# Performance work log

Hardware: AMD Instinct MI355X
Metric: run time of the kernel (lower is better)

The kernel has to match this reference:

```python
import jax, jax.numpy as jnp
import numpy as np

N = 100000
E = 1600000
FEAT = 128
EMB = 64
HID = 64
OUT = 16


def _glorot(key, shape):
    fan_in, fan_out = shape[1], shape[0]
    lim = (6.0 / (fan_in + fan_out)) ** 0.5
    return jax.random.uniform(key, shape, jnp.float32, -lim, lim)


def setup_inputs() -> dict:
    key = jax.random.key(0)
    ks = jax.random.split(key, 16)
    return {
        "x_feat": jax.random.normal(ks[0], (N, FEAT), jnp.float32),
        "x_emb": jax.random.normal(ks[1], (N, 2, EMB), jnp.float32),
        "edge_index": jax.random.randint(ks[2], (2, E), 0, N, jnp.int32),
        # layer 0: SAGEConv(FEAT -> HID), Linear(EMB -> HID)
        "Wl0": _glorot(ks[3], (HID, FEAT)),
        "bl0": jnp.zeros((HID,), jnp.float32),
        "Wr0": _glorot(ks[4], (HID, FEAT)),
        "We0": _glorot(ks[5], (HID, EMB)),
        "be0": jnp.zeros((HID,), jnp.float32),
        # layer 1 (last): SAGEConv(HID -> OUT), Linear(EMB==HID -> OUT)
        "Wl1": _glorot(ks[6], (OUT, HID)),
        "bl1": jnp.zeros((OUT,), jnp.float32),
        "Wr1": _glorot(ks[7], (OUT, HID)),
        "We1": _glorot(ks[8], (OUT, HID)),
        "be1": jnp.zeros((OUT,), jnp.float32),
    }


def _sage_conv(x, edge_index, Wl, bl, Wr):
    # PyG SAGEConv with mean aggregation:
    #   out = lin_l(mean_{j in N(i)} x_j) + lin_r(x_i)
    src, dst = edge_index[0], edge_index[1]
    msg = x[src]                                   # [E, C] gather
    agg = jax.ops.segment_sum(msg, dst, num_segments=N)       # [N, C]
    deg = jax.ops.segment_sum(jnp.ones((E,), x.dtype), dst, num_segments=N)
    agg = agg / jnp.maximum(deg, 1.0)[:, None]     # mean over neighbors
    return agg @ Wl.T + bl + x @ Wr.T


def reference(x_feat, x_emb, edge_index,
              Wl0, bl0, Wr0, We0, be0,
              Wl1, bl1, Wr1, We1, be1):
    # forward(x=(x_feat, x_emb), edge_index=...) path, eval mode (dropout p=0)
    e = x_emb.mean(axis=1)                         # [N, EMB]
    # layer 0 (all but last): relu(sage + linear(emb))
    h = _sage_conv(x_feat, edge_index, Wl0, bl0, Wr0)
    e = e @ We0.T + be0
    h = jax.nn.relu(h + e)
    # last layer: no relu
    h = _sage_conv(h, edge_index, Wl1, bl1, Wr1)
    e = e @ We1.T + be1
    return h + e
```

## Files before the change

kernel.cpp:

```cpp
#include <hip/hip_runtime.h>
#include <hip/hip_bf16.h>
#include <cstddef>

#define NN 100000
#define EE 1600000
#define NPB 128
#define NB  782
#define ECH 4096
#define NCH 391
#define CAP 4096

typedef __attribute__((ext_vector_type(8))) short bf16x8;
typedef __attribute__((ext_vector_type(8))) unsigned short u16x8;
typedef __attribute__((ext_vector_type(4))) float f32x4;

#define YTS 72

static inline int ceil_div(int a, int b){ return (a + b - 1) / b; }

__device__ inline unsigned short f2bf(float f){
  union { float f; unsigned u; } v; v.f = f;
  unsigned r = (v.u + 0x7fff + ((v.u >> 16) & 1)) >> 16;
  return (unsigned short)r;
}
__device__ inline float bf2f(unsigned short s){
  union { unsigned u; float f; } v; v.u = ((unsigned)s) << 16;
  return v.f;
}

#define PRE_W (128 * 192)
#define PRE_E (PRE_W + 16 * 64)
#define PRE_B (PRE_E + 16)
#define PRE_C (PRE_B + 64)
#define PRE_N (PRE_C + NB)
__global__ void prep_all_kernel(const float* __restrict__ Wl0, const float* __restrict__ Wr0,
                                const float* __restrict__ We0, const float* __restrict__ bl0,
                                const float* __restrict__ be0, const float* __restrict__ We1,
                                const float* __restrict__ be1,
                                unsigned short* __restrict__ wcat, float* __restrict__ wee,
                                float* __restrict__ b1e, float* __restrict__ bias0,
                                int* __restrict__ cur){
  int idx = blockIdx.x * blockDim.x + threadIdx.x;
  if (idx < PRE_W){
    int n = idx / 192, k = idx % 192;
    float v;
    if (n < 64) v = (k < 128) ? Wl0[n * 128 + k] : 0.f;
    else        v = (k < 128) ? Wr0[(n - 64) * 128 + k] : We0[(n - 64) * 64 + (k - 128)];
    wcat[idx] = f2bf(v);
  } else if (idx < PRE_E){
    int j = idx - PRE_W;
    int i = j >> 6, c = j & 63;
    float s = 0.f;
    for (int k = 0; k < 64; k++) s += We1[i * 64 + k] * We0[k * 64 + c];
    wee[j] = s;
  } else if (idx < PRE_B){
    int i = idx - PRE_E;
    float s = be1[i];
    for (int k = 0; k < 64; k++) s += We1[i * 64 + k] * be0[k];
    b1e[i] = s;
  } else if (idx < PRE_C){
    int i = idx - PRE_B;
    bias0[i] = bl0[i] + be0[i];
  } else if (idx < PRE_N){
    cur[idx - PRE_C] = 0;
  }
}

__global__ __launch_bounds__(256) void escatter_kernel(const int* __restrict__ src,
                                                       const int* __restrict__ dst,
                                                       int* __restrict__ cur,
                                                       int* __restrict__ ebkt){
  __shared__ int lh[NB];
  __shared__ int lo[NB];
  int t = threadIdx.x;
  int e0 = blockIdx.x * ECH;
  int ne = EE - e0; if (ne > ECH) ne = ECH;
  for (int i = t; i < NB; i += 256) lh[i] = 0;
  __syncthreads();
  for (int i = t; i < ne; i += 256)
    atomicAdd(&lh[dst[e0 + i] >> 7], 1);
  __syncthreads();
  for (int i = t; i < NB; i += 256){
    int c = lh[i];
    lo[i] = c ? atomicAdd(&cur[i], c) : 0;
    lh[i] = 0;
  }
  __syncthreads();
  for (int i = t; i < ne; i += 256){
    int d = dst[e0 + i], b = d >> 7;
    int r = atomicAdd(&lh[b], 1);
    int p = lo[b] + r;
    if (p < CAP) ebkt[b * CAP + p] = ((d & 127) << 24) | src[e0 + i];
  }
}

__global__ __launch_bounds__(256) void bsort_kernel(
    const int* __restrict__ cur, int* __restrict__ ebkt,
    int* __restrict__ rs, int* __restrict__ deg){
  __shared__ int lraw[CAP];
  __shared__ int lout[CAP];
  __shared__ int lh[NPB];
  __shared__ int loff[NPB];
  __shared__ int lcur[NPB];
  const int t = threadIdx.x;
  const int b = blockIdx.x;
  const int e0 = b * CAP;
  int cnt = cur[b];
  if (cnt > CAP) cnt = CAP;
  for (int i = t; i < NPB; i += 256) lh[i] = 0;
  __syncthreads();
  for (int i = t; i < cnt; i += 256){
    int w = ebkt[e0 + i];
    lraw[i] = w;
    atomicAdd(&lh[((unsigned)w) >> 24], 1);
  }
  __syncthreads();
  {
    int v = (t < NPB) ? lh[t] : 0;
    int s = v;
    for (int off = 1; off < NPB; off <<= 1){
      int x = 0;
      if (t < NPB && t >= off) x = loff[t - off];
      __syncthreads();
      if (t < NPB) loff[t] = s;
      __syncthreads();
      if (t < NPB && t >= off) s += loff[t - off];
      __syncthreads();
    }
    if (t < NPB){ loff[t] = s - v; lcur[t] = s - v; }
  }
  __syncthreads();
  for (int i = t; i < cnt; i += 256){
    int w = lraw[i];
    int d = ((unsigned)w) >> 24;
    int pos = atomicAdd(&lcur[d], 1);
    lout[pos] = w & 0xFFFFFF;
  }
  __syncthreads();
  for (int i = t; i < cnt; i += 256) ebkt[e0 + i] = lout[i];
  if (t < NPB){
    int node = b * NPB + t;
    if (node < NN){
      rs[node]  = e0 + loff[t];
      deg[node] = lh[t];
    }
  }
}

__global__ __launch_bounds__(256, 4) void l0_gemm_kernel(
    const float* __restrict__ x_feat, const float* __restrict__ x_emb,
    const unsigned short* __restrict__ wcat,
    unsigned short* __restrict__ y0g, unsigned short* __restrict__ re0g,
    unsigned short* __restrict__ e_bf, int M){
  __shared__ unsigned short smem[64 * 200];
  unsigned short* As = smem;
  unsigned short* Ys = smem;
  unsigned short* Rs = smem + 64 * YTS;
  const int t = threadIdx.x;
  const int row0 = blockIdx.x * 64;
  float4 tmpa[12], tmpb[12];
  #pragma unroll
  for (int k = 0; k < 12; k++){
    int idx = t + k * 256;
    int r = idx / 48, q = idx % 48;
    int row = row0 + r;
    float4 v = make_float4(0.f, 0.f, 0.f, 0.f);
    float4 u = make_float4(0.f, 0.f, 0.f, 0.f);
    if (row < M){
      if (q < 32) v = ((const float4*)x_feat)[(size_t)row * 32 + q];
      else {
        v = ((const float4*)x_emb)[(size_t)row * 32 + (q - 32)];
        u = ((const float4*)x_emb)[(size_t)row * 32 + 16 + (q - 32)];
      }
    }
    tmpa[k] = v; tmpb[k] = u;
  }
  #pragma unroll
  for (int k = 0; k < 12; k++){
    int idx = t + k * 256;
    int r = idx / 48, q = idx % 48;
    int row = row0 + r;
    float4 v = tmpa[k];
    if (q >= 32){
      float4 u = tmpb[k];
      v.x = 0.5f * (v.x + u.x); v.y = 0.5f * (v.y + u.y);
      v.z = 0.5f * (v.z + u.z); v.w = 0.5f * (v.w + u.w);
    }
    ushort4 s; s.x = f2bf(v.x); s.y = f2bf(v.y); s.z = f2bf(v.z); s.w = f2bf(v.w);
    *(ushort4*)&As[r * 200 + q * 4] = s;
    if (q >= 32 && row < M)
      *(ushort4*)&e_bf[(size_t)row * 64 + (q - 32) * 4] = s;
  }
  const int w = t >> 6, l = t & 63;
  const int lm = l & 15, quad = l >> 4;
  bf16x8 bfr0[6], bfr1[6];
  {
    int n0 = w * 16 + lm;
    int n1 = 64 + w * 16 + lm;
    #pragma unroll
    for (int ks = 0; ks < 6; ks++){
      bfr0[ks] = *(const bf16x8*)&wcat[n0 * 192 + ks * 32 + quad * 8];
      bfr1[ks] = *(const bf16x8*)&wcat[n1 * 192 + ks * 32 + quad * 8];
    }
  }
  __syncthreads();
  f32x4 a0[4], a1[4];
  #pragma unroll
  for (int rg = 0; rg < 4; rg++){
    bf16x8 af[6];
    #pragma unroll
    for (int ks = 0; ks < 6; ks++)
      af[ks] = *(const bf16x8*)&As[(rg * 16 + lm) * 200 + ks * 32 + quad * 8];
    f32x4 acc0 = {0.f, 0.f, 0.f, 0.f};
    f32x4 acc1 = {0.f, 0.f, 0.f, 0.f};
    #pragma unroll
    for (int ks = 0; ks < 6; ks++){
      acc0 = __builtin_amdgcn_mfma_f32_16x16x32_bf16(af[ks], bfr0[ks], acc0, 0, 0, 0);
      acc1 = __builtin_amdgcn_mfma_f32_16x16x32_bf16(af[ks], bfr1[ks], acc1, 0, 0, 0);
    }
    a0[rg] = acc0; a1[rg] = acc1;
  }
  __syncthreads();
  #pragma unroll
  for (int rg = 0; rg < 4; rg++){
    #pragma unroll
    for (int r = 0; r < 4; r++){
      int lrow = rg * 16 + quad * 4 + r;
      Ys[lrow * YTS + w * 16 + lm] = f2bf(a0[rg][r]);
      Rs[lrow * YTS + w * 16 + lm] = f2bf(a1[rg][r]);
    }
  }
  __syncthreads();
  #pragma unroll
  for (int k = 0; k < 2; k++){
    int idx = t + k * 256;
    int r = idx >> 3, c8 = idx & 7;
    int grow = row0 + r;
    if (grow < M){
      *(u16x8*)&y0g[(size_t)grow * 64 + c8 * 8]  = *(const u16x8*)&Ys[r * YTS + c8 * 8];
      *(u16x8*)&re0g[(size_t)grow * 64 + c8 * 8] = *(const u16x8*)&Rs[r * YTS + c8 * 8];
    }
  }
}

__global__ void agg0_kernel(const unsigned short* __restrict__ y0,
                            const unsigned short* __restrict__ re0,
                            const float* __restrict__ bias0,
                            const int* __restrict__ rs, const int* __restrict__ deg,
                            const int* __restrict__ ssrc, unsigned short* __restrict__ h){
  int g = blockIdx.x * blockDim.x + threadIdx.x;
  if (g >= NN * 8) return;
  int node = g >> 3, lane = g & 7;
  int start = rs[node], cnt = deg[node];
  float acc[4][8] = {};
  int i = 0;
  for (; i + 8 <= cnt; i += 8){
    int s[8];
    #pragma unroll
    for (int j = 0; j < 8; j++) s[j] = ssrc[start + i + j];
    u16x8 v[8];
    #pragma unroll
    for (int j = 0; j < 8; j++) v[j] = *(const u16x8*)&y0[(size_t)s[j] * 64 + lane * 8];
    #pragma unroll
    for (int j = 0; j < 8; j++)
      #pragma unroll
      for (int k = 0; k < 8; k++) acc[j & 3][k] += bf2f((unsigned short)v[j][k]);
  }
  for (; i < cnt; i++){
    int s = ssrc[start + i];
    u16x8 v = *(const u16x8*)&y0[(size_t)s * 64 + lane * 8];
    #pragma unroll
    for (int k = 0; k < 8; k++) acc[0][k] += bf2f((unsigned short)v[k]);
  }
  float inv = 1.0f / (float)(cnt > 1 ? cnt : 1);
  u16x8 rv = *(const u16x8*)&re0[(size_t)node * 64 + lane * 8];
  float4 ba = ((const float4*)bias0)[lane * 2];
  float4 bb = ((const float4*)bias0)[lane * 2 + 1];
  float bv[8] = {ba.x, ba.y, ba.z, ba.w, bb.x, bb.y, bb.z, bb.w};
  u16x8 o;
  #pragma unroll
  for (int k = 0; k < 8; k++){
    float sum = (acc[0][k] + acc[1][k]) + (acc[2][k] + acc[3][k]);
    float x = sum * inv + bf2f((unsigned short)rv[k]) + bv[k];
    o[k] = f2bf(x > 0.f ? x : 0.f);
  }
  *(u16x8*)&h[(size_t)node * 64 + lane * 8] = o;
}

__global__ __launch_bounds__(256) void gemm16_dual_kernel(
    const unsigned short* __restrict__ H, const unsigned short* __restrict__ E,
    const float* __restrict__ Wl1, const float* __restrict__ Wr1,
    const float* __restrict__ wee,
    const float* __restrict__ bl1, const float* __restrict__ b1e,
    unsigned short* __restrict__ Y1, float* __restrict__ Out, int M){
  __shared__ float Hs[64][65];
  __shared__ float Es[64][65];
  __shared__ float Wls[16][65];
  __shared__ float Wrs[16][65];
  __shared__ float Wes[16][65];
  __shared__ float bs[16];
  const int t = threadIdx.x;
  const int row0 = blockIdx.x * 64;
  {
    int j = t >> 4, kq = t & 15;
    float4 a = ((const float4*)Wl1)[j * 16 + kq];
    float4 b = ((const float4*)Wr1)[j * 16 + kq];
    float4 c = ((const float4*)wee)[j * 16 + kq];
    Wls[j][kq*4+0]=a.x; Wls[j][kq*4+1]=a.y; Wls[j][kq*4+2]=a.z; Wls[j][kq*4+3]=a.w;
    Wrs[j][kq*4+0]=b.x; Wrs[j][kq*4+1]=b.y; Wrs[j][kq*4+2]=b.z; Wrs[j][kq*4+3]=b.w;
    Wes[j][kq*4+0]=c.x; Wes[j][kq*4+1]=c.y; Wes[j][kq*4+2]=c.z; Wes[j][kq*4+3]=c.w;
  }
  if (t < 16) bs[t] = bl1[t] + b1e[t];
  for (int idx = t; idx < 64 * 16; idx += 256){
    int n = idx >> 4, kq = idx & 15;
    int row = row0 + n;
    ushort4 hv = make_ushort4(0,0,0,0), ev = make_ushort4(0,0,0,0);
    if (row < M){
      hv = *(const ushort4*)&H[(size_t)row * 64 + kq * 4];
      ev = *(const ushort4*)&E[(size_t)row * 64 + kq * 4];
    }
    Hs[n][kq*4+0]=bf2f(hv.x); Hs[n][kq*4+1]=bf2f(hv.y); Hs[n][kq*4+2]=bf2f(hv.z); Hs[n][kq*4+3]=bf2f(hv.w);
    Es[n][kq*4+0]=bf2f(ev.x); Es[n][kq*4+1]=bf2f(ev.y); Es[n][kq*4+2]=bf2f(ev.z); Es[n][kq*4+3]=bf2f(ev.w);
  }
  __syncthreads();
  const int n = t >> 2, jq = t & 3;
  float y[4] = {}, o[4] = {};
  #pragma unroll 4
  for (int k = 0; k < 64; k++){
    float a = Hs[n][k];
    float e = Es[n][k];
    #pragma unroll
    for (int j = 0; j < 4; j++){
      y[j] = fmaf(a, Wls[jq*4 + j][k], y[j]);
      o[j] = fmaf(a, Wrs[jq*4 + j][k], o[j]);
      o[j] = fmaf(e, Wes[jq*4 + j][k], o[j]);
    }
  }
  int row = row0 + n;
  if (row < M){
    ushort4 yb; yb.x = f2bf(y[0]); yb.y = f2bf(y[1]); yb.z = f2bf(y[2]); yb.w = f2bf(y[3]);
    *(ushort4*)&Y1[(size_t)row * 16 + jq * 4] = yb;
    ((float4*)Out)[(size_t)row * 4 + jq] =
        make_float4(o[0] + bs[jq*4+0], o[1] + bs[jq*4+1], o[2] + bs[jq*4+2], o[3] + bs[jq*4+3]);
  }
}

__global__ void agg1_kernel(const unsigned short* __restrict__ y1,
                            const int* __restrict__ rs, const int* __restrict__ deg,
                            const int* __restrict__ ssrc, float* __restrict__ outp){
  int g = blockIdx.x * blockDim.x + threadIdx.x;
  if (g >= NN * 2) return;
  int node = g >> 1, lane = g & 1;
  int start = rs[node], cnt = deg[node];
  float acc[4][8] = {};
  int i = 0;
  for (; i + 8 <= cnt; i += 8){
    int s[8];
    #pragma unroll
    for (int j = 0; j < 8; j++) s[j] = ssrc[start + i + j];
    u16x8 v[8];
    #pragma unroll
    for (int j = 0; j < 8; j++) v[j] = *(const u16x8*)&y1[(size_t)s[j] * 16 + lane * 8];
    #pragma unroll
    for (int j = 0; j < 8; j++)
      #pragma unroll
      for (int k = 0; k < 8; k++) acc[j & 3][k] += bf2f((unsigned short)v[j][k]);
  }
  for (; i < cnt; i++){
    int s = ssrc[start + i];
    u16x8 v = *(const u16x8*)&y1[(size_t)s * 16 + lane * 8];
    #pragma unroll
    for (int k = 0; k < 8; k++) acc[0][k] += bf2f((unsigned short)v[k]);
  }
  float inv = 1.0f / (float)(cnt > 1 ? cnt : 1);
  f32x4 o0 = *(f32x4*)&outp[(size_t)node * 16 + lane * 8];
  f32x4 o1 = *(f32x4*)&outp[(size_t)node * 16 + lane * 8 + 4];
  #pragma unroll
  for (int k = 0; k < 4; k++){
    o0[k] += ((acc[0][k] + acc[1][k]) + (acc[2][k] + acc[3][k])) * inv;
    o1[k] += ((acc[0][k+4] + acc[1][k+4]) + (acc[2][k+4] + acc[3][k+4])) * inv;
  }
  *(f32x4*)&outp[(size_t)node * 16 + lane * 8]     = o0;
  *(f32x4*)&outp[(size_t)node * 16 + lane * 8 + 4] = o1;
}

extern "C" void kernel_launch(void* const* d_in, const int* in_sizes, int n_in,
                              void* d_out, int out_size, void* d_ws, size_t ws_size,
                              hipStream_t stream){
  (void)in_sizes; (void)n_in; (void)out_size; (void)ws_size;
  const float* x_feat = (const float*)d_in[0];
  const float* x_emb  = (const float*)d_in[1];
  const int*   ei     = (const int*)d_in[2];
  const float* Wl0 = (const float*)d_in[3];
  const float* bl0 = (const float*)d_in[4];
  const float* Wr0 = (const float*)d_in[5];
  const float* We0 = (const float*)d_in[6];
  const float* be0 = (const float*)d_in[7];
  const float* Wl1 = (const float*)d_in[8];
  const float* bl1 = (const float*)d_in[9];
  const float* Wr1 = (const float*)d_in[10];
  const float* We1 = (const float*)d_in[11];
  const float* be1 = (const float*)d_in[12];
  float* out = (float*)d_out;

  char* w = (char*)d_ws;
  unsigned short* re0 = (unsigned short*)w;  w += sizeof(unsigned short) * (size_t)NN * 64;
  unsigned short* h   = (unsigned short*)w;  w += sizeof(unsigned short) * (size_t)NN * 64;
  unsigned short* y0  = (unsigned short*)w;  w += sizeof(unsigned short) * (size_t)NN * 64;
  unsigned short* e_bf= (unsigned short*)w;  w += sizeof(unsigned short) * (size_t)NN * 64;
  unsigned short* y1  = (unsigned short*)w;  w += sizeof(unsigned short) * (size_t)NN * 16;
  unsigned short* wcat= (unsigned short*)w;  w += sizeof(unsigned short) * 128 * 192;
  float* wee   = (float*)w;                  w += sizeof(float) * 16 * 64;
  float* b1e   = (float*)w;                  w += sizeof(float) * 16;
  float* bias0 = (float*)w;                  w += sizeof(float) * 64;
  int* ebkt    = (int*)w;                    w += sizeof(int) * (size_t)NB * CAP;
  int* cur     = (int*)w;                    w += sizeof(int) * NB;
  int* rs      = (int*)w;                    w += sizeof(int) * NN;
  int* deg     = (int*)w;                    w += sizeof(int) * NN;

  const int* srcp = ei;
  const int* dstp = ei + EE;

  prep_all_kernel<<<ceil_div(PRE_N, 256), 256, 0, stream>>>(
      Wl0, Wr0, We0, bl0, be0, We1, be1, wcat, wee, b1e, bias0, cur);

  escatter_kernel<<<NCH, 256, 0, stream>>>(srcp, dstp, cur, ebkt);
  bsort_kernel<<<NB, 256, 0, stream>>>(cur, ebkt, rs, deg);

  l0_gemm_kernel<<<ceil_div(NN, 64), 256, 0, stream>>>(x_feat, x_emb, wcat, y0, re0, e_bf, NN);

  agg0_kernel<<<ceil_div(NN * 8, 256), 256, 0, stream>>>(
      y0, re0, bias0, rs, deg, ebkt, h);

  gemm16_dual_kernel<<<ceil_div(NN, 64), 256, 0, stream>>>(h, e_bf, Wl1, Wr1, wee,
                                                           bl1, b1e, y1, out, NN);
  agg1_kernel<<<ceil_div(NN * 2, 256), 256, 0, stream>>>(y1, rs, deg, ebkt, out);
}
```

Measured before the change: 328.4 us.

## Pre-convert inputs to bf16 in separate kernel, keep root term in fp32

Adds an xprep kernel that converts x_feat and the averaged x_emb into one packed bf16 buffer. The layer-0 GEMM then loads bf16 rows directly, and the layer-1 GEMM reads the embedding slice from that buffer, which removes the separate e_bf array. The root-term output re0 is now stored as fp32 instead of bf16, with a separate shared-memory tile, and occupancy drops from 4 to 3 blocks. escatter preloads its dst indices into registers so the two histogram passes do not read them twice. The cost is an extra full pass writing 38 MB of bf16 input and doubled bytes for re0.

Result: faster. 310.2 us (-5.5%).

```diff
diff --git a/kernel.cpp b/kernel.cpp
--- a/kernel.cpp
+++ b/kernel.cpp
@@ -15,6 +15,7 @@
 typedef __attribute__((ext_vector_type(4))) float f32x4;
 
 #define YTS 72
+#define RTS 68
 
 static inline int ceil_div(int a, int b){ return (a + b - 1) / b; }
 
@@ -66,6 +67,31 @@
   }
 }
 
+__global__ void xprep_kernel(const float* __restrict__ xf, const float* __restrict__ xe,
+                             unsigned short* __restrict__ xb){
+  int g = blockIdx.x * blockDim.x + threadIdx.x;
+  if (g >= NN * 24) return;
+  int node = g / 24, c8 = g % 24;
+  u16x8 o;
+  if (c8 < 16){
+    float4 a = ((const float4*)xf)[(size_t)node * 32 + c8 * 2];
+    float4 b = ((const float4*)xf)[(size_t)node * 32 + c8 * 2 + 1];
+    o[0]=f2bf(a.x); o[1]=f2bf(a.y); o[2]=f2bf(a.z); o[3]=f2bf(a.w);
+    o[4]=f2bf(b.x); o[5]=f2bf(b.y); o[6]=f2bf(b.z); o[7]=f2bf(b.w);
+  } else {
+    int q = c8 - 16;
+    float4 a0 = ((const float4*)xe)[(size_t)node * 32 + q * 2];
+    float4 a1 = ((const float4*)xe)[(size_t)node * 32 + q * 2 + 1];
+    float4 b0 = ((const float4*)xe)[(size_t)node * 32 + 16 + q * 2];
+    float4 b1 = ((const float4*)xe)[(size_t)node * 32 + 16 + q * 2 + 1];
+    o[0]=f2bf(0.5f*(a0.x+b0.x)); o[1]=f2bf(0.5f*(a0.y+b0.y));
+    o[2]=f2bf(0.5f*(a0.z+b0.z)); o[3]=f2bf(0.5f*(a0.w+b0.w));
+    o[4]=f2bf(0.5f*(a1.x+b1.x)); o[5]=f2bf(0.5f*(a1.y+b1.y));
+    o[6]=f2bf(0.5f*(a1.z+b1.z)); o[7]=f2bf(0.5f*(a1.w+b1.w));
+  }
+  *(u16x8*)&xb[(size_t)node * 192 + c8 * 8] = o;
+}
+
 __global__ __launch_bounds__(256) void escatter_kernel(const int* __restrict__ src,
                                                        const int* __restrict__ dst,
                                                        int* __restrict__ cur,
@@ -77,8 +103,15 @@
   int ne = EE - e0; if (ne > ECH) ne = ECH;
   for (int i = t; i < NB; i += 256) lh[i] = 0;
   __syncthreads();
-  for (int i = t; i < ne; i += 256)
-    atomicAdd(&lh[dst[e0 + i] >> 7], 1);
+  int dl[16];
+  #pragma unroll
+  for (int k = 0; k < 16; k++){
+    int i = t + k * 256;
+    dl[k] = (i < ne) ? dst[e0 + i] : -1;
+  }
+  #pragma unroll
+  for (int k = 0; k < 16; k++)
+    if (dl[k] >= 0) atomicAdd(&lh[dl[k] >> 7], 1);
   __syncthreads();
   for (int i = t; i < NB; i += 256){
     int c = lh[i];
@@ -86,11 +119,15 @@
     lh[i] = 0;
   }
   __syncthreads();
-  for (int i = t; i < ne; i += 256){
-    int d = dst[e0 + i], b = d >> 7;
-    int r = atomicAdd(&lh[b], 1);
-    int p = lo[b] + r;
-    if (p < CAP) ebkt[b * CAP + p] = ((d & 127) << 24) | src[e0 + i];
+  #pragma unroll
+  for (int k = 0; k < 16; k++){
+    int i = t + k * 256;
+    if (dl[k] >= 0){
+      int d = dl[k], b = d >> 7;
+      int r = atomicAdd(&lh[b], 1);
+      int p = lo[b] + r;
+      if (p < CAP) ebkt[b * CAP + p] = ((d & 127) << 24) | src[e0 + i];
+    }
   }
 }
 
@@ -147,49 +184,28 @@
   }
 }
 
-__global__ __launch_bounds__(256, 4) void l0_gemm_kernel(
-    const float* __restrict__ x_feat, const float* __restrict__ x_emb,
-    const unsigned short* __restrict__ wcat,
-    unsigned short* __restrict__ y0g, unsigned short* __restrict__ re0g,
-    unsigned short* __restrict__ e_bf, int M){
-  __shared__ unsigned short smem[64 * 200];
-  unsigned short* As = smem;
-  unsigned short* Ys = smem;
-  unsigned short* Rs = smem + 64 * YTS;
+__global__ __launch_bounds__(256, 3) void l0_gemm_kernel(
+    const unsigned short* __restrict__ xb, const unsigned short* __restrict__ wcat,
+    unsigned short* __restrict__ y0g, float* __restrict__ re0g, int M){
+  __shared__ unsigned short As[64 * 200];
+  __shared__ unsigned short Ys[64 * YTS];
+  __shared__ float          Rs[64 * RTS];
   const int t = threadIdx.x;
   const int row0 = blockIdx.x * 64;
-  float4 tmpa[12], tmpb[12];
-  #pragma unroll
-  for (int k = 0; k < 12; k++){
+  u16x8 tmp[6];
+  #pragma unroll
+  for (int k = 0; k < 6; k++){
     int idx = t + k * 256;
-    int r = idx / 48, q = idx % 48;
+    int r = idx / 24, q = idx % 24;
     int row = row0 + r;
-    float4 v = make_float4(0.f, 0.f, 0.f, 0.f);
-    float4 u = make_float4(0.f, 0.f, 0.f, 0.f);
-    if (row < M){
-      if (q < 32) v = ((const float4*)x_feat)[(size_t)row * 32 + q];
-      else {
-        v = ((const float4*)x_emb)[(size_t)row * 32 + (q - 32)];
-        u = ((const float4*)x_emb)[(size_t)row * 32 + 16 + (q - 32)];
-      }
-    }
-    tmpa[k] = v; tmpb[k] = u;
-  }
-  #pragma unroll
-  for (int k = 0; k < 12; k++){
+    u16x8 z = {0,0,0,0,0,0,0,0};
+    tmp[k] = (row < M) ? *(const u16x8*)&xb[(size_t)row * 192 + q * 8] : z;
+  }
+  #pragma unroll
+  for (int k = 0; k < 6; k++){
     int idx = t + k * 256;
-    int r = idx / 48, q = idx % 48;
-    int row = row0 + r;
-    float4 v = tmpa[k];
-    if (q >= 32){
-      float4 u = tmpb[k];
-      v.x = 0.5f * (v.x + u.x); v.y = 0.5f * (v.y + u.y);
-      v.z = 0.5f * (v.z + u.z); v.w = 0.5f * (v.w + u.w);
-    }
-    ushort4 s; s.x = f2bf(v.x); s.y = f2bf(v.y); s.z = f2bf(v.z); s.w = f2bf(v.w);
-    *(ushort4*)&As[r * 200 + q * 4] = s;
-    if (q >= 32 && row < M)
-      *(ushort4*)&e_bf[(size_t)row * 64 + (q - 32) * 4] = s;
+    int r = idx / 24, q = idx % 24;
+    *(u16x8*)&As[r * 200 + q * 8] = tmp[k];
   }
   const int w = t >> 6, l = t & 63;
   const int lm = l & 15, quad = l >> 4;
@@ -204,8 +220,6 @@
     }
   }
   __syncthreads();
-  f32x4 a0[4], a1[4];
-  #pragma unroll
   for (int rg = 0; rg < 4; rg++){
     bf16x8 af[6];
     #pragma unroll
@@ -218,16 +232,11 @@
       acc0 = __builtin_amdgcn_mfma_f32_16x16x32_bf16(af[ks], bfr0[ks], acc0, 0, 0, 0);
       acc1 = __builtin_amdgcn_mfma_f32_16x16x32_bf16(af[ks], bfr1[ks], acc1, 0, 0, 0);
     }
-    a0[rg] = acc0; a1[rg] = acc1;
-  }
-  __syncthreads();
-  #pragma unroll
-  for (int rg = 0; rg < 4; rg++){
     #pragma unroll
     for (int r = 0; r < 4; r++){
       int lrow = rg * 16 + quad * 4 + r;
-      Ys[lrow * YTS + w * 16 + lm] = f2bf(a0[rg][r]);
-      Rs[lrow * YTS + w * 16 + lm] = f2bf(a1[rg][r]);
+      Ys[lrow * YTS + w * 16 + lm] = f2bf(acc0[r]);
+      Rs[lrow * RTS + w * 16 + lm] = acc1[r];
     }
   }
   __syncthreads();
@@ -236,15 +245,21 @@
     int idx = t + k * 256;
     int r = idx >> 3, c8 = idx & 7;
     int grow = row0 + r;
-    if (grow < M){
-      *(u16x8*)&y0g[(size_t)grow * 64 + c8 * 8]  = *(const u16x8*)&Ys[r * YTS + c8 * 8];
-      *(u16x8*)&re0g[(size_t)grow * 64 + c8 * 8] = *(const u16x8*)&Rs[r * YTS + c8 * 8];
-    }
+    if (grow < M)
+      *(u16x8*)&y0g[(size_t)grow * 64 + c8 * 8] = *(const u16x8*)&Ys[r * YTS + c8 * 8];
+  }
+  #pragma unroll
+  for (int k = 0; k < 4; k++){
+    int idx = t + k * 256;
+    int r = idx >> 4, c4 = idx & 15;
+    int grow = row0 + r;
+    if (grow < M)
+      *(f32x4*)&re0g[(size_t)grow * 64 + c4 * 4] = *(const f32x4*)&Rs[r * RTS + c4 * 4];
   }
 }
 
 __global__ void agg0_kernel(const unsigned short* __restrict__ y0,
-                            const unsigned short* __restrict__ re0,
+                            const float* __restrict__ re0,
                             const float* __restrict__ bias0,
                             const int* __restrict__ rs, const int* __restrict__ deg,
                             const int* __restrict__ ssrc, unsigned short* __restrict__ h){
@@ -273,7 +288,9 @@
     for (int k = 0; k < 8; k++) acc[0][k] += bf2f((unsigned short)v[k]);
   }
   float inv = 1.0f / (float)(cnt > 1 ? cnt : 1);
-  u16x8 rv = *(const u16x8*)&re0[(size_t)node * 64 + lane * 8];
+  f32x4 rv0 = *(const f32x4*)&re0[(size_t)node * 64 + lane * 8];
+  f32x4 rv1 = *(const f32x4*)&re0[(size_t)node * 64 + lane * 8 + 4];
+  float rvv[8] = {rv0[0], rv0[1], rv0[2], rv0[3], rv1[0], rv1[1], rv1[2], rv1[3]};
   float4 ba = ((const float4*)bias0)[lane * 2];
   float4 bb = ((const float4*)bias0)[lane * 2 + 1];
   float bv[8] = {ba.x, ba.y, ba.z, ba.w, bb.x, bb.y, bb.z, bb.w};
@@ -281,14 +298,14 @@
   #pragma unroll
   for (int k = 0; k < 8; k++){
     float sum = (acc[0][k] + acc[1][k]) + (acc[2][k] + acc[3][k]);
-    float x = sum * inv + bf2f((unsigned short)rv[k]) + bv[k];
+    float x = sum * inv + rvv[k] + bv[k];
     o[k] = f2bf(x > 0.f ? x : 0.f);
   }
   *(u16x8*)&h[(size_t)node * 64 + lane * 8] = o;
 }
 
 __global__ __launch_bounds__(256) void gemm16_dual_kernel(
-    const unsigned short* __restrict__ H, const unsigned short* __restrict__ E,
+    const unsigned short* __restrict__ H, const unsigned short* __restrict__ xb,
     const float* __restrict__ Wl1, const float* __restrict__ Wr1,
     const float* __restrict__ wee,
     const float* __restrict__ bl1, const float* __restrict__ b1e,
@@ -317,7 +334,7 @@
     ushort4 hv = make_ushort4(0,0,0,0), ev = make_ushort4(0,0,0,0);
     if (row < M){
       hv = *(const ushort4*)&H[(size_t)row * 64 + kq * 4];
-      ev = *(const ushort4*)&E[(size_t)row * 64 + kq * 4];
+      ev = *(const ushort4*)&xb[(size_t)row * 192 + 128 + kq * 4];
     }
     Hs[n][kq*4+0]=bf2f(hv.x); Hs[n][kq*4+1]=bf2f(hv.y); Hs[n][kq*4+2]=bf2f(hv.z); Hs[n][kq*4+3]=bf2f(hv.w);
     Es[n][kq*4+0]=bf2f(ev.x); Es[n][kq*4+1]=bf2f(ev.y); Es[n][kq*4+2]=bf2f(ev.z); Es[n][kq*4+3]=bf2f(ev.w);
@@ -404,10 +421,10 @@
   float* out = (float*)d_out;
 
   char* w = (char*)d_ws;
-  unsigned short* re0 = (unsigned short*)w;  w += sizeof(unsigned short) * (size_t)NN * 64;
+  float* re0          = (float*)w;           w += sizeof(float) * (size_t)NN * 64;
+  unsigned short* xb  = (unsigned short*)w;  w += sizeof(unsigned short) * (size_t)NN * 192;
   unsigned short* h   = (unsigned short*)w;  w += sizeof(unsigned short) * (size_t)NN * 64;
   unsigned short* y0  = (unsigned short*)w;  w += sizeof(unsigned short) * (size_t)NN * 64;
-  unsigned short* e_bf= (unsigned short*)w;  w += sizeof(unsigned short) * (size_t)NN * 64;
   unsigned short* y1  = (unsigned short*)w;  w += sizeof(unsigned short) * (size_t)NN * 16;
   unsigned short* wcat= (unsigned short*)w;  w += sizeof(unsigned short) * 128 * 192;
   float* wee   = (float*)w;                  w += sizeof(float) * 16 * 64;
@@ -424,15 +441,17 @@
   prep_all_kernel<<<ceil_div(PRE_N, 256), 256, 0, stream>>>(
       Wl0, Wr0, We0, bl0, be0, We1, be1, wcat, wee, b1e, bias0, cur);
 
+  xprep_kernel<<<ceil_div(NN * 24, 256), 256, 0, stream>>>(x_feat, x_emb, xb);
+
   escatter_kernel<<<NCH, 256, 0, stream>>>(srcp, dstp, cur, ebkt);
   bsort_kernel<<<NB, 256, 0, stream>>>(cur, ebkt, rs, deg);
 
-  l0_gemm_kernel<<<ceil_div(NN, 64), 256, 0, stream>>>(x_feat, x_emb, wcat, y0, re0, e_bf, NN);
+  l0_gemm_kernel<<<ceil_div(NN, 64), 256, 0, stream>>>(xb, wcat, y0, re0, NN);
 
   agg0_kernel<<<ceil_div(NN * 8, 256), 256, 0, stream>>>(
       y0, re0, bias0, rs, deg, ebkt, h);
 
-  gemm16_dual_kernel<<<ceil_div(NN, 64), 256, 0, stream>>>(h, e_bf, Wl1, Wr1, wee,
+  gemm16_dual_kernel<<<ceil_div(NN, 64), 256, 0, stream>>>(h, xb, Wl1, Wr1, wee,
                                                            bl1, b1e, y1, out, NN);
   agg1_kernel<<<ceil_div(NN * 2, 256), 256, 0, stream>>>(y1, rs, deg, ebkt, out);
 }
```
